# Kernel tuning notes

Measured on AMD Instinct MI355X. Metric: run time of the kernel, lower is better.

The kernel has to match this reference:

```python
import jax, jax.numpy as jnp
import numpy as np

B, S, DIM = 4, 1024, 4096
HQ, HKV, HD = 32, 8, 128
MAX_SEQ = 2048
START_POS = 1024
THETA = 10000.0


def _rope_tables(start, seqlen, head_dim, theta):
    inv = 1.0 / (theta ** (np.arange(0, head_dim, 2, dtype=np.float32) / head_dim))
    pos = np.arange(start, start + seqlen, dtype=np.float32)
    ang = np.outer(pos, inv)  # [S, HD/2]
    return jnp.asarray(np.cos(ang)), jnp.asarray(np.sin(ang))


def setup_inputs() -> dict:
    key = jax.random.key(0)
    ks = jax.random.split(key, 8)
    sc = 1.0 / np.sqrt(DIM)
    x = jax.random.normal(ks[0], (B, S, DIM), jnp.float32)
    wq = jax.random.normal(ks[1], (DIM, HQ * HD), jnp.float32) * sc
    wk = jax.random.normal(ks[2], (DIM, HKV * HD), jnp.float32) * sc
    wv = jax.random.normal(ks[3], (DIM, HKV * HD), jnp.float32) * sc
    wo = jax.random.normal(ks[4], (HQ * HD, DIM), jnp.float32) * sc
    cache_k = jax.random.normal(ks[5], (B, MAX_SEQ, HKV, HD), jnp.float32)
    cache_v = jax.random.normal(ks[6], (B, MAX_SEQ, HKV, HD), jnp.float32)
    cos, sin = _rope_tables(START_POS, S, HD, THETA)
    return {"x": x, "wq": wq, "wk": wk, "wv": wv, "wo": wo,
            "freqs_cos": cos, "freqs_sin": sin,
            "cache_k": cache_k, "cache_v": cache_v, "start_pos": START_POS}


def _apply_rope(t, cos, sin):
    # t: [B, S, H, HD]; cos/sin: [S, HD/2]
    b, s, h, d = t.shape
    tr = t.reshape(b, s, h, d // 2, 2)
    xr, xi = tr[..., 0], tr[..., 1]
    c = cos[None, :, None, :]
    sn = sin[None, :, None, :]
    outr = xr * c - xi * sn
    outi = xr * sn + xi * c
    return jnp.stack([outr, outi], axis=-1).reshape(b, s, h, d)


def reference(x, wq, wk, wv, wo, freqs_cos, freqs_sin, cache_k, cache_v, start_pos):
    b, s, _ = x.shape
    rep = HQ // HKV
    q = (x @ wq).reshape(b, s, HQ, HD)
    k = (x @ wk).reshape(b, s, HKV, HD)
    v = (x @ wv).reshape(b, s, HKV, HD)
    q = _apply_rope(q, freqs_cos, freqs_sin)
    k = _apply_rope(k, freqs_cos, freqs_sin)
    # write new K/V into the cache at start_pos (static int -> static slice)
    cache_k = cache_k.at[:, start_pos:start_pos + s].set(k)
    cache_v = cache_v.at[:, start_pos:start_pos + s].set(v)
    keys = cache_k[:, : start_pos + s]     # [B, KV, HKV, HD]
    values = cache_v[:, : start_pos + s]
    # GQA: group query heads with their KV head instead of materializing repeat_kv
    qg = q.reshape(b, s, HKV, rep, HD)
    scores = jnp.einsum('bqhrd,bkhd->bhrqk', qg, keys) / jnp.sqrt(
        jnp.asarray(HD, x.dtype))
    probs = jax.nn.softmax(scores, axis=-1).astype(x.dtype)
    out = jnp.einsum('bhrqk,bkhd->bqhrd', probs, values)
    out = out.reshape(b, s, HQ * HD)
    return out @ wo
```

## Files before the change

### kernel.cpp

```cpp
#include <hip/hip_runtime.h>

typedef _Float16 half_t;
typedef _Float16 half8 __attribute__((ext_vector_type(8)));
typedef _Float16 half4v __attribute__((ext_vector_type(4)));
typedef _Float16 half2v __attribute__((ext_vector_type(2)));
typedef float floatx4 __attribute__((ext_vector_type(4)));

#define TOK 4096
#define DIM 4096
#define S_LEN 1024
#define B_SZ 4
#define HQ_N 32
#define HKV_N 8
#define HD_N 128
#define L_KV 2048
#define NKV 1024
#define NKV2 2048
#define QK_SCALE 0.08838834764831845f

__device__ __forceinline__ void gload_lds16(const void* g, void* l) {
  __builtin_amdgcn_global_load_lds(
      (const __attribute__((address_space(1))) unsigned int*)g,
      (__attribute__((address_space(3))) unsigned int*)l, 16, 0, 0);
}

__global__ __launch_bounds__(256) void conv_x_kernel(const float* __restrict__ x,
                                                     half_t* __restrict__ xh) {
  int t = blockIdx.x * 256 + threadIdx.x;
  floatx4 v = *((const floatx4*)x + t);
  half4v o;
  o[0] = (half_t)v[0]; o[1] = (half_t)v[1]; o[2] = (half_t)v[2]; o[3] = (half_t)v[3];
  *((half4v*)xh + t) = o;
}

__global__ __launch_bounds__(256) void conv_transpose(const float* __restrict__ in,
                                                      half_t* __restrict__ out,
                                                      int K, int N) {
  __shared__ half_t T[64 * 65];
  const int tid = threadIdx.x;
  const int n0 = blockIdx.x * 64, k0 = blockIdx.y * 64;
  #pragma unroll
  for (int i = 0; i < 16; ++i) {
    int idx = i * 256 + tid;
    int r = idx >> 6, c = idx & 63;
    T[c * 65 + r] = (half_t)in[(size_t)(k0 + r) * N + n0 + c];
  }
  __syncthreads();
  #pragma unroll
  for (int i = 0; i < 16; ++i) {
    int idx = i * 256 + tid;
    int rn = idx >> 6, ck = idx & 63;
    out[(size_t)(n0 + rn) * K + k0 + ck] = T[rn * 65 + ck];
  }
}

template <typename OT>
__global__ __launch_bounds__(256) void gemm_f16(const half_t* __restrict__ A,
                                                const half_t* __restrict__ BT,
                                                OT* __restrict__ C,
                                                int M, int N, int K) {
  __shared__ half_t As[128 * 32];
  __shared__ half_t Bs[128 * 32];
  const int tid = threadIdx.x;
  const int lane = tid & 63;
  const int w = tid >> 6;
  const int wr = w >> 1, wc = w & 1;
  const int g = lane >> 4, qr = lane & 15;
  const int m0 = blockIdx.y * 128, n0 = blockIdx.x * 128;
  floatx4 acc[4][4] = {};
  const int chb0 = tid & 192;
  for (int k0 = 0; k0 < K; k0 += 32) {
    #pragma unroll
    for (int i = 0; i < 2; ++i) {
      int chb = chb0 + 256 * i;
      int ch = chb + lane;
      int row = ch >> 2, c8 = ch & 3;
      gload_lds16(A + (size_t)(m0 + row) * K + k0 + c8 * 8, (char*)As + chb * 16);
      gload_lds16(BT + (size_t)(n0 + row) * K + k0 + c8 * 8, (char*)Bs + chb * 16);
    }
    __syncthreads();
    half8 af[4], bf[4];
    const int koff = g * 8;
    #pragma unroll
    for (int m = 0; m < 4; ++m)
      af[m] = *(const half8*)&As[(wr * 64 + m * 16 + qr) * 32 + koff];
    #pragma unroll
    for (int n = 0; n < 4; ++n)
      bf[n] = *(const half8*)&Bs[(wc * 64 + n * 16 + qr) * 32 + koff];
    #pragma unroll
    for (int m = 0; m < 4; ++m)
      #pragma unroll
      for (int n = 0; n < 4; ++n)
        acc[m][n] = __builtin_amdgcn_mfma_f32_16x16x32_f16(af[m], bf[n], acc[m][n], 0, 0, 0);
    __syncthreads();
  }
  #pragma unroll
  for (int m = 0; m < 4; ++m) {
    int rb = m0 + wr * 64 + m * 16 + g * 4;
    #pragma unroll
    for (int n = 0; n < 4; ++n) {
      int col = n0 + wc * 64 + n * 16 + qr;
      #pragma unroll
      for (int r = 0; r < 4; ++r)
        C[(size_t)(rb + r) * N + col] = (OT)acc[m][n][r];
    }
  }
}

template <typename OT>
__global__ __launch_bounds__(512) void gemm256(const half_t* __restrict__ A,
                                               const half_t* __restrict__ BT,
                                               OT* __restrict__ C,
                                               int M, int N, int K) {
  __shared__ __align__(16) char smem[131072];
  const int tid = threadIdx.x;
  const int lane = tid & 63, w = tid >> 6;
  const int g = lane >> 4, qr = lane & 15;
  const int wm = w >> 2, wn = w & 3;
  const int nbx = N >> 8;
  const int nwg = gridDim.x;
  const int cpx = nwg >> 3;
  const int bid = ((int)blockIdx.x & 7) * cpx + ((int)blockIdx.x >> 3);
  const int bx = bid % nbx, by = bid / nbx;
  const int m0 = by << 8, n0 = bx << 8;
  const int NT = K >> 6;

  const int ch0 = tid, ch1 = tid + 512;
  const int sr0 = ch0 >> 3, sc0 = (ch0 & 7) ^ (sr0 & 7);
  const int sr1 = ch1 >> 3, sc1 = (ch1 & 7) ^ (sr1 & 7);
  const size_t so0 = (size_t)sr0 * K + sc0 * 8;
  const size_t so1 = (size_t)sr1 * K + sc1 * 8;
  const int wb = (w * 64) * 16;
  const half_t* Ab = A + (size_t)m0 * K;
  const half_t* Bb = BT + (size_t)n0 * K;

#define G_STAGE(gsrc, ldst)                                   \
  do {                                                        \
    gload_lds16((gsrc) + so0, (char*)(ldst) + wb);            \
    gload_lds16((gsrc) + so1, (char*)(ldst) + wb + 8192);     \
  } while (0)

#define FRAG(base, row, kb) \
  (*(const half8*)((base) + ((((row) * 128) + (kb)) ^ (((row) & 7) << 4))))

  G_STAGE(Ab, smem);
  G_STAGE(Ab + (size_t)128 * K, smem + 16384);
  G_STAGE(Bb, smem + 65536);
  G_STAGE(Bb + (size_t)128 * K, smem + 81920);
  G_STAGE(Ab + 64, smem + 32768);
  G_STAGE(Bb + 64, smem + 98304);
  asm volatile("s_waitcnt vmcnt(4)" ::: "memory");
  __builtin_amdgcn_s_barrier();

  floatx4 acc[8][4] = {};
  half8 aF[4][2], bF0[2][2], bF1[2][2];

#define MFMA_Q(mh, nh, BF)                                                     \
  do {                                                                         \
    __builtin_amdgcn_s_setprio(1);                                             \
    _Pragma("unroll") for (int mf = 0; mf < 4; ++mf)                           \
    _Pragma("unroll") for (int nf = 0; nf < 2; ++nf)                           \
    _Pragma("unroll") for (int kk = 0; kk < 2; ++kk)                           \
      acc[(mh)*4 + mf][(nh)*2 + nf] = __builtin_amdgcn_mfma_f32_16x16x32_f16(  \
          aF[mf][kk], BF[nf][kk], acc[(mh)*4 + mf][(nh)*2 + nf], 0, 0, 0);     \
    __builtin_amdgcn_s_setprio(0);                                             \
  } while (0)

  for (int t = 0; t < NT; ++t) {
    const char* Ac = smem + ((t & 1) ? 32768 : 0);
    const char* Bc = smem + 65536 + ((t & 1) ? 32768 : 0);
    char* An = smem + ((t & 1) ? 0 : 32768);
    char* Bn = smem + 65536 + ((t & 1) ? 0 : 32768);
    const int t1 = (t + 1 < NT) ? t + 1 : NT - 1;
    const int t2 = (t + 2 < NT) ? t + 2 : NT - 1;
    #pragma unroll
    for (int mf = 0; mf < 4; ++mf)
      #pragma unroll
      for (int kk = 0; kk < 2; ++kk)
        aF[mf][kk] = FRAG(Ac, wm * 128 + mf * 16 + qr, kk * 64 + g * 16);
    #pragma unroll
    for (int nf = 0; nf < 2; ++nf)
      #pragma unroll
      for (int kk = 0; kk < 2; ++kk)
        bF0[nf][kk] = FRAG(Bc, wn * 64 + nf * 16 + qr, kk * 64 + g * 16);
    G_STAGE(Ab + (size_t)128 * K + t1 * 64, An + 16384);
    __builtin_amdgcn_s_barrier();
    asm volatile("s_waitcnt lgkmcnt(0)" ::: "memory");
    MFMA_Q(0, 0, bF0);
    __builtin_amdgcn_s_barrier();
    #pragma unroll
    for (int nf = 0; nf < 2; ++nf)
      #pragma unroll
      for (int kk = 0; kk < 2; ++kk)
        bF1[nf][kk] = FRAG(Bc, wn * 64 + 32 + nf * 16 + qr, kk * 64 + g * 16);
    G_STAGE(Bb + (size_t)128 * K + t1 * 64, Bn + 16384);
    __builtin_amdgcn_s_barrier();
    asm volatile("s_waitcnt lgkmcnt(0)" ::: "memory");
    MFMA_Q(0, 1, bF1);
    __builtin_amdgcn_s_barrier();
    #pragma unroll
    for (int mf = 0; mf < 4; ++mf)
      #pragma unroll
      for (int kk = 0; kk < 2; ++kk)
        aF[mf][kk] = FRAG(Ac, wm * 128 + 64 + mf * 16 + qr, kk * 64 + g * 16);
    __builtin_amdgcn_s_barrier();
    asm volatile("s_waitcnt lgkmcnt(0)" ::: "memory");
    MFMA_Q(1, 1, bF1);
    __builtin_amdgcn_s_barrier();
    G_STAGE(Ab + (size_t)t2 * 64, (char*)Ac);
    G_STAGE(Bb + (size_t)t2 * 64, (char*)Bc);
    __builtin_amdgcn_s_barrier();
    MFMA_Q(1, 0, bF0);
    asm volatile("s_waitcnt vmcnt(4)" ::: "memory");
    __builtin_amdgcn_s_barrier();
  }
  #pragma unroll
  for (int mh = 0; mh < 2; ++mh)
    #pragma unroll
    for (int mf = 0; mf < 4; ++mf) {
      const int rb = m0 + wm * 128 + mh * 64 + mf * 16 + g * 4;
      #pragma unroll
      for (int nh = 0; nh < 2; ++nh)
        #pragma unroll
        for (int nf = 0; nf < 2; ++nf) {
          const int col = n0 + wn * 64 + nh * 32 + nf * 16 + qr;
          floatx4 v = acc[mh * 4 + mf][nh * 2 + nf];
          #pragma unroll
          for (int r = 0; r < 4; ++r)
            C[(size_t)(rb + r) * N + col] = (OT)v[r];
        }
    }
#undef G_STAGE
#undef FRAG
#undef MFMA_Q
}

__global__ __launch_bounds__(256) void pack_q_kernel(const half_t* __restrict__ qf,
                                                     const float* __restrict__ cosT,
                                                     const float* __restrict__ sinT,
                                                     half_t* __restrict__ qh) {
  int t = blockIdx.x * 256 + threadIdx.x;
  int j = t & 63;
  int hq = (t >> 6) & 31;
  int tok = t >> 11;
  int s = tok & 1023;
  int b = tok >> 10;
  const half_t* src = qf + (size_t)tok * DIM + hq * HD_N + 2 * j;
  float xr = (float)src[0], xi = (float)src[1];
  float c = cosT[s * 64 + j], sn = sinT[s * 64 + j];
  half2v o;
  o[0] = (half_t)((xr * c - xi * sn) * QK_SCALE);
  o[1] = (half_t)((xr * sn + xi * c) * QK_SCALE);
  *(half2v*)(qh + ((size_t)((b * HQ_N + hq) * S_LEN + s)) * HD_N + 2 * j) = o;
}

__global__ __launch_bounds__(256) void pack_k_kernel(const half_t* __restrict__ kvf,
                                                     const float* __restrict__ cache_k,
                                                     const float* __restrict__ cosT,
                                                     const float* __restrict__ sinT,
                                                     half_t* __restrict__ kh) {
  int t = blockIdx.x * 256 + threadIdx.x;
  int j = t & 63;
  int h = (t >> 6) & 7;
  int pos = (t >> 9) & 2047;
  int b = t >> 20;
  float xr, xi;
  if (pos < 1024) {
    const float* src = cache_k + ((size_t)(b * L_KV + pos) * HKV_N + h) * HD_N + 2 * j;
    xr = src[0]; xi = src[1];
  } else {
    int s = pos - 1024;
    const half_t* src = kvf + (size_t)(b * S_LEN + s) * NKV2 + h * HD_N + 2 * j;
    float r0 = (float)src[0], i0 = (float)src[1];
    float c = cosT[s * 64 + j], sn = sinT[s * 64 + j];
    xr = r0 * c - i0 * sn;
    xi = r0 * sn + i0 * c;
  }
  half2v o; o[0] = (half_t)xr; o[1] = (half_t)xi;
  *(half2v*)(kh + ((size_t)(b * HKV_N + h) * L_KV + pos) * HD_N + 2 * j) = o;
}

__global__ __launch_bounds__(256) void pack_vt_kernel(const half_t* __restrict__ kvf,
                                                      const float* __restrict__ cache_v,
                                                      half_t* __restrict__ vt) {
  __shared__ half_t T[128 * 129];
  const int tid = threadIdx.x;
  const int blk = blockIdx.x;
  const int pt = blk & 15;
  const int h = (blk >> 4) & 7;
  const int b = blk >> 7;
  const int p0 = pt * 128;
  #pragma unroll
  for (int i = 0; i < 64; ++i) {
    int idx = i * 256 + tid;
    int p = idx >> 7, d = idx & 127;
    int pos = p0 + p;
    float v;
    if (pos < 1024)
      v = cache_v[((size_t)(b * L_KV + pos) * HKV_N + h) * HD_N + d];
    else
      v = (float)kvf[(size_t)(b * S_LEN + (pos - 1024)) * NKV2 + NKV + h * HD_N + d];
    T[d * 129 + p] = (half_t)v;
  }
  __syncthreads();
  #pragma unroll
  for (int i = 0; i < 64; ++i) {
    int idx = i * 256 + tid;
    int d = idx >> 7, p = idx & 127;
    vt[((size_t)(b * HKV_N + h) * HD_N + d) * L_KV + p0 + p] = T[d * 129 + p];
  }
}

__global__ __launch_bounds__(256) void attn_kernel(const half_t* __restrict__ qh,
                                                   const half_t* __restrict__ kh,
                                                   const half_t* __restrict__ vt,
                                                   half_t* __restrict__ ah) {
  __shared__ __align__(16) half_t K2[2][64 * 128];
  __shared__ __align__(16) half_t V2[2][128 * 64];
  __shared__ __align__(16) half_t Pl[4][16 * 72];
  const int tid = threadIdx.x;
  const int lane = tid & 63, w = tid >> 6;
  const int g = lane >> 4, qr = lane & 15;
  const int qt = blockIdx.x, hq = blockIdx.y, b = blockIdx.z;
  const int hkv = hq >> 2;
  const half_t* qbase =
      qh + ((size_t)((b * HQ_N + hq) * S_LEN) + qt * 64 + w * 16 + qr) * HD_N;
  half8 qf[4];
  #pragma unroll
  for (int c = 0; c < 4; ++c) qf[c] = *(const half8*)(qbase + g * 8 + c * 32);
  floatx4 acc[8] = {};
  float m_run = -1e30f, l_run = 0.f;
  const half_t* kg = kh + (size_t)(b * HKV_N + hkv) * L_KV * HD_N;
  const half_t* vg = vt + (size_t)(b * HKV_N + hkv) * HD_N * L_KV;

#define STAGE_KV(kt, kb)                                                        \
  do {                                                                          \
    _Pragma("unroll") for (int i = 0; i < 4; ++i) {                             \
      int ch = tid + 256 * i;                                                   \
      int row = ch >> 4;                                                        \
      int c8 = (ch & 15) ^ (row & 7);                                           \
      gload_lds16(kg + (size_t)((kt)*64 + row) * HD_N + c8 * 8,                 \
                  (char*)K2[kb] + (tid & ~63) * 16 + i * 4096);                 \
    }                                                                           \
    _Pragma("unroll") for (int i = 0; i < 4; ++i) {                             \
      int ch = tid + 256 * i;                                                   \
      int d = ch >> 3;                                                          \
      int p8 = (ch & 7) ^ (d & 7);                                              \
      gload_lds16(vg + (size_t)d * L_KV + (kt)*64 + p8 * 8,                     \
                  (char*)V2[kb] + (tid & ~63) * 16 + i * 4096);                 \
    }                                                                           \
  } while (0)

  STAGE_KV(0, 0);
  asm volatile("s_waitcnt vmcnt(0)" ::: "memory");
  __builtin_amdgcn_s_barrier();

  for (int kt = 0; kt < L_KV / 64; ++kt) {
    const int cb = kt & 1;
    if (kt + 1 < L_KV / 64) STAGE_KV(kt + 1, cb ^ 1);
    const char* Kt = (const char*)K2[cb];
    const char* Vt = (const char*)V2[cb];
    float sc[16];
    __builtin_amdgcn_s_setprio(1);
    #pragma unroll
    for (int ts = 0; ts < 4; ++ts) {
      floatx4 tq = {0.f, 0.f, 0.f, 0.f};
      #pragma unroll
      for (int c = 0; c < 4; ++c) {
        int row = ts * 16 + qr;
        int lb = (row * 256 + (g * 8 + c * 32) * 2) ^ ((row & 7) << 4);
        half8 kfr = *(const half8*)(Kt + lb);
        tq = __builtin_amdgcn_mfma_f32_16x16x32_f16(kfr, qf[c], tq, 0, 0, 0);
      }
      sc[ts * 4 + 0] = tq[0]; sc[ts * 4 + 1] = tq[1];
      sc[ts * 4 + 2] = tq[2]; sc[ts * 4 + 3] = tq[3];
    }
    __builtin_amdgcn_s_setprio(0);
    float pmax = sc[0];
    #pragma unroll
    for (int j = 1; j < 16; ++j) pmax = fmaxf(pmax, sc[j]);
    pmax = fmaxf(pmax, __shfl_xor(pmax, 16, 64));
    pmax = fmaxf(pmax, __shfl_xor(pmax, 32, 64));
    const bool skip = __all(pmax - m_run <= 8.f);
    float mnew = skip ? m_run : fmaxf(m_run, pmax);
    float rs = 0.f;
    #pragma unroll
    for (int j = 0; j < 16; ++j) {
      float p = __expf(sc[j] - mnew);
      sc[j] = p;
      rs += p;
    }
    rs += __shfl_xor(rs, 16, 64);
    rs += __shfl_xor(rs, 32, 64);
    if (skip) {
      l_run += rs;
    } else {
      float scale = __expf(m_run - mnew);
      l_run = l_run * scale + rs;
      float f0 = __shfl(scale, g * 4 + 0, 64);
      float f1 = __shfl(scale, g * 4 + 1, 64);
      float f2 = __shfl(scale, g * 4 + 2, 64);
      float f3 = __shfl(scale, g * 4 + 3, 64);
      #pragma unroll
      for (int n = 0; n < 8; ++n) {
        acc[n][0] *= f0; acc[n][1] *= f1; acc[n][2] *= f2; acc[n][3] *= f3;
      }
      m_run = mnew;
    }
    #pragma unroll
    for (int ts = 0; ts < 4; ++ts) {
      half4v p4;
      p4[0] = (half_t)sc[ts * 4 + 0]; p4[1] = (half_t)sc[ts * 4 + 1];
      p4[2] = (half_t)sc[ts * 4 + 2]; p4[3] = (half_t)sc[ts * 4 + 3];
      *(half4v*)&Pl[w][qr * 72 + ts * 16 + g * 4] = p4;
    }
    __builtin_amdgcn_s_setprio(1);
    #pragma unroll
    for (int kc = 0; kc < 2; ++kc) {
      half8 pf = *(const half8*)&Pl[w][qr * 72 + kc * 32 + g * 8];
      #pragma unroll
      for (int n = 0; n < 8; ++n) {
        int d = n * 16 + qr;
        int lb = (d * 128 + (kc * 32 + g * 8) * 2) ^ ((d & 7) << 4);
        half8 vfr = *(const half8*)(Vt + lb);
        acc[n] = __builtin_amdgcn_mfma_f32_16x16x32_f16(pf, vfr, acc[n], 0, 0, 0);
      }
    }
    __builtin_amdgcn_s_setprio(0);
    asm volatile("s_waitcnt vmcnt(0)" ::: "memory");
    __builtin_amdgcn_s_barrier();
  }
  float il0 = 1.f / __shfl(l_run, g * 4 + 0, 64);
  float il1 = 1.f / __shfl(l_run, g * 4 + 1, 64);
  float il2 = 1.f / __shfl(l_run, g * 4 + 2, 64);
  float il3 = 1.f / __shfl(l_run, g * 4 + 3, 64);
  const int tokb = b * S_LEN + qt * 64 + w * 16 + g * 4;
  #pragma unroll
  for (int n = 0; n < 8; ++n) {
    const int col = hq * HD_N + n * 16 + qr;
    ah[(size_t)(tokb + 0) * DIM + col] = (half_t)(acc[n][0] * il0);
    ah[(size_t)(tokb + 1) * DIM + col] = (half_t)(acc[n][1] * il1);
    ah[(size_t)(tokb + 2) * DIM + col] = (half_t)(acc[n][2] * il2);
    ah[(size_t)(tokb + 3) * DIM + col] = (half_t)(acc[n][3] * il3);
  }
#undef STAGE_KV
}

extern "C" void kernel_launch(void* const* d_in, const int* in_sizes, int n_in,
                              void* d_out, int out_size, void* d_ws, size_t ws_size,
                              hipStream_t stream) {
  (void)in_sizes; (void)n_in; (void)out_size; (void)ws_size;
  const float* x = (const float*)d_in[0];
  const float* wq = (const float*)d_in[1];
  const float* wk = (const float*)d_in[2];
  const float* wv = (const float*)d_in[3];
  const float* wo = (const float*)d_in[4];
  const float* fc = (const float*)d_in[5];
  const float* fs = (const float*)d_in[6];
  const float* ck = (const float*)d_in[7];
  const float* cv = (const float*)d_in[8];

  char* ws = (char*)d_ws;
  size_t off = 0;
  auto alloc = [&](size_t bytes) {
    char* p = ws + off;
    off += (bytes + 255) & ~(size_t)255;
    return p;
  };
  half_t* xh    = (half_t*)alloc((size_t)TOK * DIM * 2);
  half_t* wqT   = (half_t*)alloc((size_t)DIM * DIM * 2);
  half_t* kvT   = (half_t*)alloc((size_t)NKV2 * DIM * 2);
  half_t* kvf16 = (half_t*)alloc((size_t)TOK * NKV2 * 2);
  half_t* qf16  = (half_t*)alloc((size_t)TOK * DIM * 2);
  half_t* kh    = (half_t*)alloc((size_t)B_SZ * HKV_N * L_KV * HD_N * 2);
  half_t* vth   = (half_t*)alloc((size_t)B_SZ * HKV_N * HD_N * L_KV * 2);
  half_t* qh    = xh;
  half_t* ah    = qf16;
  half_t* woT   = kvT;

  conv_x_kernel<<<dim3(TOK * DIM / 4 / 256), dim3(256), 0, stream>>>(x, xh);
  conv_transpose<<<dim3(DIM / 64, DIM / 64), dim3(256), 0, stream>>>(wq, wqT, DIM, DIM);
  conv_transpose<<<dim3(NKV / 64, DIM / 64), dim3(256), 0, stream>>>(wk, kvT, DIM, NKV);
  conv_transpose<<<dim3(NKV / 64, DIM / 64), dim3(256), 0, stream>>>(wv, kvT + (size_t)NKV * DIM, DIM, NKV);
  gemm256<half_t><<<dim3((TOK / 256) * (DIM / 256)), dim3(512), 0, stream>>>(xh, wqT, qf16, TOK, DIM, DIM);
  gemm_f16<half_t><<<dim3(NKV2 / 128, TOK / 128), dim3(256), 0, stream>>>(xh, kvT, kvf16, TOK, NKV2, DIM);
  pack_q_kernel<<<dim3(B_SZ * S_LEN * HQ_N * 64 / 256), dim3(256), 0, stream>>>(qf16, fc, fs, qh);
  pack_k_kernel<<<dim3(B_SZ * L_KV * HKV_N * 64 / 256), dim3(256), 0, stream>>>(kvf16, ck, fc, fs, kh);
  pack_vt_kernel<<<dim3(B_SZ * HKV_N * (L_KV / 128)), dim3(256), 0, stream>>>(kvf16, cv, vth);
  attn_kernel<<<dim3(S_LEN / 64, HQ_N, B_SZ), dim3(256), 0, stream>>>(qh, kh, vth, ah);
  conv_transpose<<<dim3(DIM / 64, DIM / 64), dim3(256), 0, stream>>>(wo, woT, DIM, DIM);
  gemm256<float><<<dim3((TOK / 256) * (DIM / 256)), dim3(512), 0, stream>>>(ah, woT, (float*)d_out, TOK, DIM, DIM);
}
```

Measured before the change: 722.7 us.

## Fuse QKV projections into one GEMM and streamline attention inner loop

Concatenates the transposed Wq/Wk/Wv weights and runs a single large gemm256 producing a fused QKV buffer, which removes the separate smaller 128-tile K/V GEMM. Pack kernels are updated to read from the fused layout. The attention kernel folds log2(e) into the Q scale so it can use raw v_exp_f32. It also precomputes swizzled LDS and global pointers, unrolls the double-buffered loop by two with constant buffer offsets, and uses packed fp16 conversion for P. The fused GEMM has a larger output buffer and the workspace aliasing is reshuffled.

```diff
diff --git a/kernel.cpp b/kernel.cpp
--- a/kernel.cpp
+++ b/kernel.cpp
@@ -15,13 +15,18 @@
 #define HD_N 128
 #define L_KV 2048
 #define NKV 1024
-#define NKV2 2048
+#define NQKV 6144
 #define QK_SCALE 0.08838834764831845f
+#define LOG2E 1.4426950408889634f
 
 __device__ __forceinline__ void gload_lds16(const void* g, void* l) {
   __builtin_amdgcn_global_load_lds(
       (const __attribute__((address_space(1))) unsigned int*)g,
       (__attribute__((address_space(3))) unsigned int*)l, 16, 0, 0);
+}
+
+__device__ __forceinline__ float max3f(float a, float b, float c) {
+  return fmaxf(fmaxf(a, b), c);
 }
 
 __global__ __launch_bounds__(256) void conv_x_kernel(const float* __restrict__ x,
@@ -51,59 +56,6 @@
     int idx = i * 256 + tid;
     int rn = idx >> 6, ck = idx & 63;
     out[(size_t)(n0 + rn) * K + k0 + ck] = T[rn * 65 + ck];
-  }
-}
-
-template <typename OT>
-__global__ __launch_bounds__(256) void gemm_f16(const half_t* __restrict__ A,
-                                                const half_t* __restrict__ BT,
-                                                OT* __restrict__ C,
-                                                int M, int N, int K) {
-  __shared__ half_t As[128 * 32];
-  __shared__ half_t Bs[128 * 32];
-  const int tid = threadIdx.x;
-  const int lane = tid & 63;
-  const int w = tid >> 6;
-  const int wr = w >> 1, wc = w & 1;
-  const int g = lane >> 4, qr = lane & 15;
-  const int m0 = blockIdx.y * 128, n0 = blockIdx.x * 128;
-  floatx4 acc[4][4] = {};
-  const int chb0 = tid & 192;
-  for (int k0 = 0; k0 < K; k0 += 32) {
-    #pragma unroll
-    for (int i = 0; i < 2; ++i) {
-      int chb = chb0 + 256 * i;
-      int ch = chb + lane;
-      int row = ch >> 2, c8 = ch & 3;
-      gload_lds16(A + (size_t)(m0 + row) * K + k0 + c8 * 8, (char*)As + chb * 16);
-      gload_lds16(BT + (size_t)(n0 + row) * K + k0 + c8 * 8, (char*)Bs + chb * 16);
-    }
-    __syncthreads();
-    half8 af[4], bf[4];
-    const int koff = g * 8;
-    #pragma unroll
-    for (int m = 0; m < 4; ++m)
-      af[m] = *(const half8*)&As[(wr * 64 + m * 16 + qr) * 32 + koff];
-    #pragma unroll
-    for (int n = 0; n < 4; ++n)
-      bf[n] = *(const half8*)&Bs[(wc * 64 + n * 16 + qr) * 32 + koff];
-    #pragma unroll
-    for (int m = 0; m < 4; ++m)
-      #pragma unroll
-      for (int n = 0; n < 4; ++n)
-        acc[m][n] = __builtin_amdgcn_mfma_f32_16x16x32_f16(af[m], bf[n], acc[m][n], 0, 0, 0);
-    __syncthreads();
-  }
-  #pragma unroll
-  for (int m = 0; m < 4; ++m) {
-    int rb = m0 + wr * 64 + m * 16 + g * 4;
-    #pragma unroll
-    for (int n = 0; n < 4; ++n) {
-      int col = n0 + wc * 64 + n * 16 + qr;
-      #pragma unroll
-      for (int r = 0; r < 4; ++r)
-        C[(size_t)(rb + r) * N + col] = (OT)acc[m][n][r];
-    }
   }
 }
 
@@ -235,7 +187,7 @@
 #undef MFMA_Q
 }
 
-__global__ __launch_bounds__(256) void pack_q_kernel(const half_t* __restrict__ qf,
+__global__ __launch_bounds__(256) void pack_q_kernel(const half_t* __restrict__ qkv,
                                                      const float* __restrict__ cosT,
                                                      const float* __restrict__ sinT,
                                                      half_t* __restrict__ qh) {
@@ -245,16 +197,17 @@
   int tok = t >> 11;
   int s = tok & 1023;
   int b = tok >> 10;
-  const half_t* src = qf + (size_t)tok * DIM + hq * HD_N + 2 * j;
+  const half_t* src = qkv + (size_t)tok * NQKV + hq * HD_N + 2 * j;
   float xr = (float)src[0], xi = (float)src[1];
   float c = cosT[s * 64 + j], sn = sinT[s * 64 + j];
+  const float QS2 = QK_SCALE * LOG2E;
   half2v o;
-  o[0] = (half_t)((xr * c - xi * sn) * QK_SCALE);
-  o[1] = (half_t)((xr * sn + xi * c) * QK_SCALE);
+  o[0] = (half_t)((xr * c - xi * sn) * QS2);
+  o[1] = (half_t)((xr * sn + xi * c) * QS2);
   *(half2v*)(qh + ((size_t)((b * HQ_N + hq) * S_LEN + s)) * HD_N + 2 * j) = o;
 }
 
-__global__ __launch_bounds__(256) void pack_k_kernel(const half_t* __restrict__ kvf,
+__global__ __launch_bounds__(256) void pack_k_kernel(const half_t* __restrict__ qkv,
                                                      const float* __restrict__ cache_k,
                                                      const float* __restrict__ cosT,
                                                      const float* __restrict__ sinT,
@@ -270,7 +223,7 @@
     xr = src[0]; xi = src[1];
   } else {
     int s = pos - 1024;
-    const half_t* src = kvf + (size_t)(b * S_LEN + s) * NKV2 + h * HD_N + 2 * j;
+    const half_t* src = qkv + (size_t)(b * S_LEN + s) * NQKV + DIM + h * HD_N + 2 * j;
     float r0 = (float)src[0], i0 = (float)src[1];
     float c = cosT[s * 64 + j], sn = sinT[s * 64 + j];
     xr = r0 * c - i0 * sn;
@@ -280,7 +233,7 @@
   *(half2v*)(kh + ((size_t)(b * HKV_N + h) * L_KV + pos) * HD_N + 2 * j) = o;
 }
 
-__global__ __launch_bounds__(256) void pack_vt_kernel(const half_t* __restrict__ kvf,
+__global__ __launch_bounds__(256) void pack_vt_kernel(const half_t* __restrict__ qkv,
                                                       const float* __restrict__ cache_v,
                                                       half_t* __restrict__ vt) {
   __shared__ half_t T[128 * 129];
@@ -299,7 +252,7 @@
     if (pos < 1024)
       v = cache_v[((size_t)(b * L_KV + pos) * HKV_N + h) * HD_N + d];
     else
-      v = (float)kvf[(size_t)(b * S_LEN + (pos - 1024)) * NKV2 + NKV + h * HD_N + d];
+      v = (float)qkv[(size_t)(b * S_LEN + (pos - 1024)) * NQKV + DIM + NKV + h * HD_N + d];
     T[d * 129 + p] = (half_t)v;
   }
   __syncthreads();
@@ -315,9 +268,7 @@
                                                    const half_t* __restrict__ kh,
                                                    const half_t* __restrict__ vt,
                                                    half_t* __restrict__ ah) {
-  __shared__ __align__(16) half_t K2[2][64 * 128];
-  __shared__ __align__(16) half_t V2[2][128 * 64];
-  __shared__ __align__(16) half_t Pl[4][16 * 72];
+  __shared__ __align__(16) char smem[74752];
   const int tid = threadIdx.x;
   const int lane = tid & 63, w = tid >> 6;
   const int g = lane >> 4, qr = lane & 15;
@@ -333,103 +284,114 @@
   const half_t* kg = kh + (size_t)(b * HKV_N + hkv) * L_KV * HD_N;
   const half_t* vg = vt + (size_t)(b * HKV_N + hkv) * HD_N * L_KV;
 
-#define STAGE_KV(kt, kb)                                                        \
-  do {                                                                          \
-    _Pragma("unroll") for (int i = 0; i < 4; ++i) {                             \
-      int ch = tid + 256 * i;                                                   \
-      int row = ch >> 4;                                                        \
-      int c8 = (ch & 15) ^ (row & 7);                                           \
-      gload_lds16(kg + (size_t)((kt)*64 + row) * HD_N + c8 * 8,                 \
-                  (char*)K2[kb] + (tid & ~63) * 16 + i * 4096);                 \
-    }                                                                           \
-    _Pragma("unroll") for (int i = 0; i < 4; ++i) {                             \
-      int ch = tid + 256 * i;                                                   \
-      int d = ch >> 3;                                                          \
-      int p8 = (ch & 7) ^ (d & 7);                                              \
-      gload_lds16(vg + (size_t)d * L_KV + (kt)*64 + p8 * 8,                     \
-                  (char*)V2[kb] + (tid & ~63) * 16 + i * 4096);                 \
-    }                                                                           \
+  const int sw = (qr & 7) << 4;
+  const char* kqkP[4];
+  #pragma unroll
+  for (int c = 0; c < 4; ++c) kqkP[c] = smem + qr * 256 + ((g * 16 + c * 64) ^ sw);
+  const char* vP[2];
+  #pragma unroll
+  for (int kc = 0; kc < 2; ++kc)
+    vP[kc] = smem + 32768 + qr * 128 + ((kc * 64 + g * 16) ^ sw);
+  char* pwP = smem + 65536 + w * 2304 + qr * 144 + g * 8;
+  const char* prP = smem + 65536 + w * 2304 + qr * 144 + g * 16;
+
+  const int r0 = tid >> 4;
+  const int c8k = (tid & 15) ^ (r0 & 7);
+  const half_t* kp[4];
+  #pragma unroll
+  for (int j = 0; j < 4; ++j) kp[j] = kg + (size_t)(r0 + 16 * j) * HD_N + c8k * 8;
+  const int d0 = tid >> 3;
+  const int p8v = (tid & 7) ^ (d0 & 7);
+  const half_t* vp[4];
+  #pragma unroll
+  for (int j = 0; j < 4; ++j) vp[j] = vg + (size_t)(d0 + 32 * j) * L_KV + p8v * 8;
+  const int ldsb = (tid & 192) * 16;
+
+#define ISSUE_STAGE(NKB)                                                     \
+  do {                                                                       \
+    _Pragma("unroll") for (int j2 = 0; j2 < 4; ++j2)                         \
+      gload_lds16(kp[j2], smem + (NKB) + ldsb + j2 * 4096);                  \
+    _Pragma("unroll") for (int j2 = 0; j2 < 4; ++j2)                         \
+      gload_lds16(vp[j2], smem + 32768 + (NKB) + ldsb + j2 * 4096);          \
+    _Pragma("unroll") for (int j2 = 0; j2 < 4; ++j2) {                       \
+      kp[j2] += 8192; vp[j2] += 64;                                          \
+    }                                                                        \
   } while (0)
 
-  STAGE_KV(0, 0);
-  asm volatile("s_waitcnt vmcnt(0)" ::: "memory");
-  __builtin_amdgcn_s_barrier();
-
-  for (int kt = 0; kt < L_KV / 64; ++kt) {
-    const int cb = kt & 1;
-    if (kt + 1 < L_KV / 64) STAGE_KV(kt + 1, cb ^ 1);
-    const char* Kt = (const char*)K2[cb];
-    const char* Vt = (const char*)V2[cb];
-    float sc[16];
-    __builtin_amdgcn_s_setprio(1);
-    #pragma unroll
-    for (int ts = 0; ts < 4; ++ts) {
-      floatx4 tq = {0.f, 0.f, 0.f, 0.f};
-      #pragma unroll
-      for (int c = 0; c < 4; ++c) {
-        int row = ts * 16 + qr;
-        int lb = (row * 256 + (g * 8 + c * 32) * 2) ^ ((row & 7) << 4);
-        half8 kfr = *(const half8*)(Kt + lb);
-        tq = __builtin_amdgcn_mfma_f32_16x16x32_f16(kfr, qf[c], tq, 0, 0, 0);
-      }
-      sc[ts * 4 + 0] = tq[0]; sc[ts * 4 + 1] = tq[1];
-      sc[ts * 4 + 2] = tq[2]; sc[ts * 4 + 3] = tq[3];
-    }
-    __builtin_amdgcn_s_setprio(0);
-    float pmax = sc[0];
-    #pragma unroll
-    for (int j = 1; j < 16; ++j) pmax = fmaxf(pmax, sc[j]);
-    pmax = fmaxf(pmax, __shfl_xor(pmax, 16, 64));
-    pmax = fmaxf(pmax, __shfl_xor(pmax, 32, 64));
-    const bool skip = __all(pmax - m_run <= 8.f);
-    float mnew = skip ? m_run : fmaxf(m_run, pmax);
-    float rs = 0.f;
-    #pragma unroll
-    for (int j = 0; j < 16; ++j) {
-      float p = __expf(sc[j] - mnew);
-      sc[j] = p;
-      rs += p;
-    }
-    rs += __shfl_xor(rs, 16, 64);
-    rs += __shfl_xor(rs, 32, 64);
-    if (skip) {
-      l_run += rs;
-    } else {
-      float scale = __expf(m_run - mnew);
-      l_run = l_run * scale + rs;
-      float f0 = __shfl(scale, g * 4 + 0, 64);
-      float f1 = __shfl(scale, g * 4 + 1, 64);
-      float f2 = __shfl(scale, g * 4 + 2, 64);
-      float f3 = __shfl(scale, g * 4 + 3, 64);
-      #pragma unroll
-      for (int n = 0; n < 8; ++n) {
-        acc[n][0] *= f0; acc[n][1] *= f1; acc[n][2] *= f2; acc[n][3] *= f3;
-      }
-      m_run = mnew;
-    }
-    #pragma unroll
-    for (int ts = 0; ts < 4; ++ts) {
-      half4v p4;
-      p4[0] = (half_t)sc[ts * 4 + 0]; p4[1] = (half_t)sc[ts * 4 + 1];
-      p4[2] = (half_t)sc[ts * 4 + 2]; p4[3] = (half_t)sc[ts * 4 + 3];
-      *(half4v*)&Pl[w][qr * 72 + ts * 16 + g * 4] = p4;
-    }
-    __builtin_amdgcn_s_setprio(1);
-    #pragma unroll
-    for (int kc = 0; kc < 2; ++kc) {
-      half8 pf = *(const half8*)&Pl[w][qr * 72 + kc * 32 + g * 8];
-      #pragma unroll
-      for (int n = 0; n < 8; ++n) {
-        int d = n * 16 + qr;
-        int lb = (d * 128 + (kc * 32 + g * 8) * 2) ^ ((d & 7) << 4);
-        half8 vfr = *(const half8*)(Vt + lb);
-        acc[n] = __builtin_amdgcn_mfma_f32_16x16x32_f16(pf, vfr, acc[n], 0, 0, 0);
-      }
-    }
-    __builtin_amdgcn_s_setprio(0);
-    asm volatile("s_waitcnt vmcnt(0)" ::: "memory");
-    __builtin_amdgcn_s_barrier();
-  }
+#define COMPUTE(KB)                                                            \
+  do {                                                                         \
+    float sc[16];                                                              \
+    __builtin_amdgcn_s_setprio(1);                                             \
+    _Pragma("unroll") for (int ts = 0; ts < 4; ++ts) {                         \
+      floatx4 tq = {0.f, 0.f, 0.f, 0.f};                                       \
+      _Pragma("unroll") for (int c = 0; c < 4; ++c)                            \
+        tq = __builtin_amdgcn_mfma_f32_16x16x32_f16(                           \
+            *(const half8*)(kqkP[c] + (KB) + ts * 4096), qf[c], tq, 0, 0, 0);  \
+      sc[ts*4+0]=tq[0]; sc[ts*4+1]=tq[1]; sc[ts*4+2]=tq[2]; sc[ts*4+3]=tq[3];  \
+    }                                                                          \
+    __builtin_amdgcn_s_setprio(0);                                             \
+    float pmax = fmaxf(                                                        \
+        max3f(max3f(sc[0], sc[1], sc[2]), max3f(sc[3], sc[4], sc[5]),          \
+              max3f(sc[6], sc[7], sc[8])),                                     \
+        max3f(max3f(sc[9], sc[10], sc[11]), max3f(sc[12], sc[13], sc[14]),     \
+              sc[15]));                                                        \
+    pmax = fmaxf(pmax, __shfl_xor(pmax, 16, 64));                              \
+    pmax = fmaxf(pmax, __shfl_xor(pmax, 32, 64));                              \
+    const bool skip = __all(pmax - m_run <= 8.f);                              \
+    const float mnew = skip ? m_run : fmaxf(m_run, pmax);                      \
+    float rs = 0.f;                                                            \
+    _Pragma("unroll") for (int j = 0; j < 16; ++j) {                           \
+      float p;                                                                 \
+      asm("v_exp_f32 %0, %1" : "=v"(p) : "v"(sc[j] - mnew));                   \
+      sc[j] = p; rs += p;                                                      \
+    }                                                                          \
+    rs += __shfl_xor(rs, 16, 64);                                              \
+    rs += __shfl_xor(rs, 32, 64);                                              \
+    if (skip) {                                                                \
+      l_run += rs;                                                             \
+    } else {                                                                   \
+      float scl;                                                               \
+      asm("v_exp_f32 %0, %1" : "=v"(scl) : "v"(m_run - mnew));                 \
+      l_run = l_run * scl + rs;                                                \
+      float f0 = __shfl(scl, g * 4 + 0, 64), f1 = __shfl(scl, g * 4 + 1, 64);  \
+      float f2 = __shfl(scl, g * 4 + 2, 64), f3 = __shfl(scl, g * 4 + 3, 64);  \
+      _Pragma("unroll") for (int n = 0; n < 8; ++n) {                          \
+        acc[n][0] *= f0; acc[n][1] *= f1; acc[n][2] *= f2; acc[n][3] *= f3;    \
+      }                                                                        \
+      m_run = mnew;                                                            \
+    }                                                                          \
+    _Pragma("unroll") for (int ts = 0; ts < 4; ++ts) {                         \
+      half2v lo = __builtin_bit_cast(                                          \
+          half2v, __builtin_amdgcn_cvt_pkrtz(sc[ts * 4 + 0], sc[ts * 4 + 1])); \
+      half2v hi = __builtin_bit_cast(                                          \
+          half2v, __builtin_amdgcn_cvt_pkrtz(sc[ts * 4 + 2], sc[ts * 4 + 3])); \
+      *(half4v*)(pwP + ts * 32) = __builtin_shufflevector(lo, hi, 0, 1, 2, 3); \
+    }                                                                          \
+    __builtin_amdgcn_s_setprio(1);                                             \
+    _Pragma("unroll") for (int kc = 0; kc < 2; ++kc) {                         \
+      half8 pf = *(const half8*)(prP + kc * 64);                               \
+      _Pragma("unroll") for (int n = 0; n < 8; ++n)                            \
+        acc[n] = __builtin_amdgcn_mfma_f32_16x16x32_f16(                       \
+            pf, *(const half8*)(vP[kc] + (KB) + n * 2048), acc[n], 0, 0, 0);   \
+    }                                                                          \
+    __builtin_amdgcn_s_setprio(0);                                             \
+  } while (0)
+
+#define ENDBAR                                          \
+  do {                                                  \
+    asm volatile("s_waitcnt vmcnt(0)" ::: "memory");    \
+    __builtin_amdgcn_s_barrier();                       \
+  } while (0)
+
+  ISSUE_STAGE(0);
+  ENDBAR;
+  for (int it = 0; it < 15; ++it) {
+    ISSUE_STAGE(16384); COMPUTE(0);     ENDBAR;
+    ISSUE_STAGE(0);     COMPUTE(16384); ENDBAR;
+  }
+  ISSUE_STAGE(16384); COMPUTE(0); ENDBAR;
+  COMPUTE(16384);
+
   float il0 = 1.f / __shfl(l_run, g * 4 + 0, 64);
   float il1 = 1.f / __shfl(l_run, g * 4 + 1, 64);
   float il2 = 1.f / __shfl(l_run, g * 4 + 2, 64);
@@ -443,7 +405,9 @@
     ah[(size_t)(tokb + 2) * DIM + col] = (half_t)(acc[n][2] * il2);
     ah[(size_t)(tokb + 3) * DIM + col] = (half_t)(acc[n][3] * il3);
   }
-#undef STAGE_KV
+#undef ISSUE_STAGE
+#undef COMPUTE
+#undef ENDBAR
 }
 
 extern "C" void kernel_launch(void* const* d_in, const int* in_sizes, int n_in,
@@ -467,26 +431,23 @@
     off += (bytes + 255) & ~(size_t)255;
     return p;
   };
-  half_t* xh    = (half_t*)alloc((size_t)TOK * DIM * 2);
-  half_t* wqT   = (half_t*)alloc((size_t)DIM * DIM * 2);
-  half_t* kvT   = (half_t*)alloc((size_t)NKV2 * DIM * 2);
-  half_t* kvf16 = (half_t*)alloc((size_t)TOK * NKV2 * 2);
-  half_t* qf16  = (half_t*)alloc((size_t)TOK * DIM * 2);
-  half_t* kh    = (half_t*)alloc((size_t)B_SZ * HKV_N * L_KV * HD_N * 2);
-  half_t* vth   = (half_t*)alloc((size_t)B_SZ * HKV_N * HD_N * L_KV * 2);
-  half_t* qh    = xh;
-  half_t* ah    = qf16;
-  half_t* woT   = kvT;
+  half_t* xh     = (half_t*)alloc((size_t)TOK * DIM * 2);
+  half_t* W      = (half_t*)alloc((size_t)NQKV * DIM * 2);
+  half_t* qkvf16 = (half_t*)alloc((size_t)TOK * NQKV * 2);
+  half_t* kh     = (half_t*)alloc((size_t)B_SZ * HKV_N * L_KV * HD_N * 2);
+  half_t* vth    = (half_t*)alloc((size_t)B_SZ * HKV_N * HD_N * L_KV * 2);
+  half_t* qh     = xh;
+  half_t* ah     = W;
+  half_t* woT    = qkvf16;
 
   conv_x_kernel<<<dim3(TOK * DIM / 4 / 256), dim3(256), 0, stream>>>(x, xh);
-  conv_transpose<<<dim3(DIM / 64, DIM / 64), dim3(256), 0, stream>>>(wq, wqT, DIM, DIM);
-  conv_transpose<<<dim3(NKV / 64, DIM / 64), dim3(256), 0, stream>>>(wk, kvT, DIM, NKV);
-  conv_transpose<<<dim3(NKV / 64, DIM / 64), dim3(256), 0, stream>>>(wv, kvT + (size_t)NKV * DIM, DIM, NKV);
-  gemm256<half_t><<<dim3((TOK / 256) * (DIM / 256)), dim3(512), 0, stream>>>(xh, wqT, qf16, TOK, DIM, DIM);
-  gemm_f16<half_t><<<dim3(NKV2 / 128, TOK / 128), dim3(256), 0, stream>>>(xh, kvT, kvf16, TOK, NKV2, DIM);
-  pack_q_kernel<<<dim3(B_SZ * S_LEN * HQ_N * 64 / 256), dim3(256), 0, stream>>>(qf16, fc, fs, qh);
-  pack_k_kernel<<<dim3(B_SZ * L_KV * HKV_N * 64 / 256), dim3(256), 0, stream>>>(kvf16, ck, fc, fs, kh);
-  pack_vt_kernel<<<dim3(B_SZ * HKV_N * (L_KV / 128)), dim3(256), 0, stream>>>(kvf16, cv, vth);
+  conv_transpose<<<dim3(DIM / 64, DIM / 64), dim3(256), 0, stream>>>(wq, W, DIM, DIM);
+  conv_transpose<<<dim3(NKV / 64, DIM / 64), dim3(256), 0, stream>>>(wk, W + (size_t)DIM * DIM, DIM, NKV);
+  conv_transpose<<<dim3(NKV / 64, DIM / 64), dim3(256), 0, stream>>>(wv, W + (size_t)(DIM + NKV) * DIM, DIM, NKV);
+  gemm256<half_t><<<dim3((TOK / 256) * (NQKV / 256)), dim3(512), 0, stream>>>(xh, W, qkvf16, TOK, NQKV, DIM);
+  pack_q_kernel<<<dim3(B_SZ * S_LEN * HQ_N * 64 / 256), dim3(256), 0, stream>>>(qkvf16, fc, fs, qh);
+  pack_k_kernel<<<dim3(B_SZ * L_KV * HKV_N * 64 / 256), dim3(256), 0, stream>>>(qkvf16, ck, fc, fs, kh);
+  pack_vt_kernel<<<dim3(B_SZ * HKV_N * (L_KV / 128)), dim3(256), 0, stream>>>(qkvf16, cv, vth);
   attn_kernel<<<dim3(S_LEN / 64, HQ_N, B_SZ), dim3(256), 0, stream>>>(qh, kh, vth, ah);
   conv_transpose<<<dim3(DIM / 64, DIM / 64), dim3(256), 0, stream>>>(wo, woT, DIM, DIM);
   gemm256<float><<<dim3((TOK / 256) * (DIM / 256)), dim3(512), 0, stream>>>(ah, woT, (float*)d_out, TOK, DIM, DIM);
```

Result: faster. 701.7 us (-2.9%).
